# Optimization experiments

Measured on AMD Instinct MI355X. Metric: run time of the kernel, lower is better.

Reference implementation:

```python
import jax, jax.numpy as jnp
import numpy as np

N_NODES = 50000
N_EDGES = 800000
D_MODEL = 128
N_HEADS = 8
D_HEAD = D_MODEL // N_HEADS  # 16
BN_EPS = 1e-5


def _batch_norm(x, gamma, beta):
    # nn.BatchNorm1d in training mode: biased batch statistics over axis 0
    mean = jnp.mean(x, axis=0)
    var = jnp.mean((x - mean) ** 2, axis=0)
    return (x - mean) * jax.lax.rsqrt(var + BN_EPS) * gamma + beta


def setup_inputs() -> dict:
    key = jax.random.key(0)
    ks = jax.random.split(key, 20)
    s = 1.0 / np.sqrt(D_MODEL)
    inp = {
        "h": jax.random.normal(ks[0], (N_NODES, D_MODEL), jnp.float32),
        "p": jax.random.normal(ks[1], (N_NODES, 16), jnp.float32),
        "e": jax.random.normal(ks[2], (N_EDGES, D_MODEL), jnp.float32),
        # attention projections (use_bias=False)
        "Wq": jax.random.normal(ks[3], (D_MODEL, D_MODEL), jnp.float32) * s,
        "Wk": jax.random.normal(ks[4], (D_MODEL, D_MODEL), jnp.float32) * s,
        "We": jax.random.normal(ks[5], (D_MODEL, D_MODEL), jnp.float32) * s,
        "Wv": jax.random.normal(ks[6], (D_MODEL, D_MODEL), jnp.float32) * s,
        # output projection O_h (bias=True)
        "Wo": jax.random.normal(ks[7], (D_MODEL, D_MODEL), jnp.float32) * s,
        "bo": jnp.zeros((D_MODEL,), jnp.float32),
        # batch norms
        "bn1_g": jnp.ones((D_MODEL,), jnp.float32),
        "bn1_b": jnp.zeros((D_MODEL,), jnp.float32),
        "bn2_g": jnp.ones((D_MODEL,), jnp.float32),
        "bn2_b": jnp.zeros((D_MODEL,), jnp.float32),
        # FFN
        "W1": jax.random.normal(ks[8], (D_MODEL, 2 * D_MODEL), jnp.float32) * s,
        "b1": jnp.zeros((2 * D_MODEL,), jnp.float32),
        "W2": jax.random.normal(ks[9], (2 * D_MODEL, D_MODEL), jnp.float32) * (1.0 / np.sqrt(2 * D_MODEL)),
        "b2": jnp.zeros((D_MODEL,), jnp.float32),
        # edge list
        "src": jax.random.randint(ks[10], (N_EDGES,), 0, N_NODES, jnp.int32),
        "dst": jax.random.randint(ks[11], (N_EDGES,), 0, N_NODES, jnp.int32),
    }
    return inp


def reference(h, p, e, Wq, Wk, We, Wv, Wo, bo, bn1_g, bn1_b, bn2_g, bn2_b,
              W1, b1, W2, b2, src, dst):
    N = h.shape[0]
    # node/edge projections -> [N,H,D] / [E,H,D]
    Qh = (h @ Wq).reshape(N, N_HEADS, D_HEAD)
    Kh = (h @ Wk).reshape(N, N_HEADS, D_HEAD)
    Vh = (h @ Wv).reshape(N, N_HEADS, D_HEAD)
    Eh = (e @ We).reshape(-1, N_HEADS, D_HEAD)
    # per-edge score: (K[src] * Q[dst]) / sqrt(d) * E  -> [E,H,D]
    score = Kh[src] * Qh[dst] / np.sqrt(D_HEAD)
    score = score * Eh
    # clamped exp of per-head sum -> [E,H,1]
    s = jnp.exp(jnp.clip(jnp.sum(score, axis=-1, keepdims=True), -5.0, 5.0))
    # scatter-sum into destination nodes
    wV = jax.ops.segment_sum(Vh[src] * s, dst, num_segments=N)  # [N,H,D]
    z = jax.ops.segment_sum(s, dst, num_segments=N)             # [N,H,1]
    h_attn = (wV / (z + 1e-6)).reshape(N, D_MODEL)
    # output projection + residual + BN (dropout=0)
    h2 = h + (h_attn @ Wo + bo)
    h2 = _batch_norm(h2, bn1_g, bn1_b)
    # FFN + residual + BN
    ffn = jax.nn.relu(h2 @ W1 + b1) @ W2 + b2
    h3 = _batch_norm(h2 + ffn, bn2_g, bn2_b)
    return h3
```

## Files before the change

kernel.cpp:

```cpp
#include <hip/hip_runtime.h>

#define DM 128
#define NH 8
#define DH 16

typedef __bf16 bf8 __attribute__((ext_vector_type(8)));
typedef __bf16 bf4 __attribute__((ext_vector_type(4)));
typedef float  f4  __attribute__((ext_vector_type(4)));

__device__ __forceinline__ f4 mfma16(bf8 a, bf8 b, f4 c){
  return __builtin_amdgcn_mfma_f32_16x16x32_bf16(a, b, c, 0, 0, 0);
}

__device__ __forceinline__ bf8 bfragT(const __bf16* __restrict__ WT, int ldk, int lane){
  const __bf16* p = WT + (size_t)(lane & 15) * ldk + ((lane >> 4) << 3);
  return *(const bf8*)p;
}

__device__ __forceinline__ bf8 cvt8(const float* __restrict__ p){
  f4 u = *(const f4*)p;
  f4 v = *(const f4*)(p + 4);
  bf8 r;
  r[0]=(__bf16)u[0]; r[1]=(__bf16)u[1]; r[2]=(__bf16)u[2]; r[3]=(__bf16)u[3];
  r[4]=(__bf16)v[0]; r[5]=(__bf16)v[1]; r[6]=(__bf16)v[2]; r[7]=(__bf16)v[3];
  return r;
}

__global__ __launch_bounds__(256) void k_prep_hist(const float* __restrict__ Wq,
    const float* __restrict__ Wk, const float* __restrict__ Wv,
    const float* __restrict__ We, const float* __restrict__ Wo,
    const float* __restrict__ W1, const float* __restrict__ W2,
    __bf16* __restrict__ WqT, __bf16* __restrict__ WkT, __bf16* __restrict__ WvT,
    __bf16* __restrict__ WeT, __bf16* __restrict__ WoT,
    __bf16* __restrict__ W1T, __bf16* __restrict__ W2T,
    const int* __restrict__ dst, int* __restrict__ deg, int E)
{
  int b = blockIdx.x;
  if (b >= 576){
    int i = (b - 576) * 256 + threadIdx.x;
    if (i < E) atomicAdd(&deg[dst[i]], 1);
    return;
  }
  const float* W; __bf16* T; int K, M, idx;
  if (b < 320){
    int w = b >> 6;
    W = w==0?Wq: w==1?Wk: w==2?Wv: w==3?We: Wo;
    T = w==0?WqT: w==1?WkT: w==2?WvT: w==3?WeT: WoT;
    K = 128; M = 128; idx = (b & 63) * 256 + threadIdx.x;
  } else if (b < 448){
    W = W1; T = W1T; K = 128; M = 256; idx = (b - 320) * 256 + threadIdx.x;
  } else {
    W = W2; T = W2T; K = 256; M = 128; idx = (b - 448) * 256 + threadIdx.x;
  }
  int m = idx / K, k = idx - m * K;
  T[idx] = (__bf16)W[(size_t)k * M + m];
}

__global__ __launch_bounds__(256) void k_scanA(const int* __restrict__ deg,
    int* __restrict__ part, int N)
{
  __shared__ int ls[256];
  int b = blockIdx.x, t = threadIdx.x;
  int i = b * 256 + t;
  ls[t] = (i < N) ? deg[i] : 0;
  __syncthreads();
  for (int d = 128; d > 0; d >>= 1){
    if (t < d) ls[t] += ls[t + d];
    __syncthreads();
  }
  if (t == 0) part[b] = ls[0];
}

__global__ __launch_bounds__(256) void k_scanB(int* __restrict__ part, int nb)
{
  __shared__ int ls[256];
  int t = threadIdx.x;
  ls[t] = (t < nb) ? part[t] : 0;
  __syncthreads();
  for (int d = 1; d < 256; d <<= 1){
    int add = (t >= d) ? ls[t - d] : 0;
    __syncthreads();
    ls[t] += add;
    __syncthreads();
  }
  if (t < nb) part[t] = (t == 0) ? 0 : ls[t - 1];
}

__global__ __launch_bounds__(256) void k_scanC(const int* __restrict__ deg,
    const int* __restrict__ part, int* __restrict__ off, int* __restrict__ cursor, int N)
{
  __shared__ int ls[256];
  int b = blockIdx.x, t = threadIdx.x;
  int i = b * 256 + t;
  int v = (i < N) ? deg[i] : 0;
  ls[t] = v;
  __syncthreads();
  for (int d = 1; d < 256; d <<= 1){
    int add = (t >= d) ? ls[t - d] : 0;
    __syncthreads();
    ls[t] += add;
    __syncthreads();
  }
  if (i < N){
    int excl = ls[t] - v + part[b];
    off[i] = excl;
    cursor[i] = excl;
  }
}

__global__ __launch_bounds__(256) void k_qkv(const float* __restrict__ h,
    const __bf16* __restrict__ WqT, const __bf16* __restrict__ WkT, const __bf16* __restrict__ WvT,
    __bf16* __restrict__ Q, __bf16* __restrict__ K, __bf16* __restrict__ V, int N)
{
  int lane = threadIdx.x & 63;
  int r0 = (blockIdx.x * 4 + (threadIdx.x >> 6)) * 16;
  if (r0 + 16 > N) return;
  bf8 a[4];
  int arow = r0 + (lane & 15);
  int koff = (lane >> 4) << 3;
#pragma unroll
  for (int kt = 0; kt < 4; ++kt)
    a[kt] = cvt8(h + (size_t)arow * DM + kt * 32 + koff);

  const __bf16* Ws[3] = {WqT, WkT, WvT};
  __bf16* Os[3] = {Q, K, V};
  int crow = r0 + ((lane >> 4) << 2);
  int ccol = lane & 15;
#pragma unroll
  for (int o = 0; o < 3; ++o){
#pragma unroll
    for (int nt = 0; nt < 8; ++nt){
      f4 acc = {0.f, 0.f, 0.f, 0.f};
#pragma unroll
      for (int kt = 0; kt < 4; ++kt)
        acc = mfma16(a[kt], bfragT(Ws[o] + (size_t)(nt * 16) * DM + kt * 32, DM, lane), acc);
      __bf16* outp = Os[o] + (size_t)crow * DM + nt * 16 + ccol;
      outp[0] = (__bf16)acc[0]; outp[DM] = (__bf16)acc[1];
      outp[2 * DM] = (__bf16)acc[2]; outp[3 * DM] = (__bf16)acc[3];
    }
  }
}

__global__ __launch_bounds__(256) void k_edge(const float* __restrict__ e,
    const __bf16* __restrict__ WeT,
    const __bf16* __restrict__ Qb, const __bf16* __restrict__ Kb,
    const int* __restrict__ src, const int* __restrict__ dst,
    int* __restrict__ cursor, int* __restrict__ sSrc, float* __restrict__ sS,
    int E, int T, int NW)
{
  __shared__ __bf16 Eh[64][132];
  int tid = threadIdx.x, lane = tid & 63, wave = tid >> 6;
  int l16 = lane & 15;
  int koff = (lane >> 4) << 3;
  int half = lane >> 5, l32 = lane & 31, hh = l32 >> 2;
  int lrow = (lane >> 4) << 2;
  int wrow = wave * 16;
  int t = blockIdx.x * 4 + wave;
  if (t >= T) return;

  int ei = min(t * 16 + l16, E - 1);
  int sv = src[ei], dv = dst[ei];
  int slotv = 0;
  if ((lane < 16) && (t * 16 + l16 < E)){
    slotv = atomicAdd(&cursor[dv], 1);
    sSrc[slotv] = sv;
  }
  f4 eu[4], ew[4];
#pragma unroll
  for (int kt = 0; kt < 4; ++kt){
    const float* p = e + (size_t)ei * DM + kt * 32 + koff;
    eu[kt] = *(const f4*)p; ew[kt] = *(const f4*)(p + 4);
  }
  bf4 kr[8], qr[8];
#pragma unroll
  for (int i = 0; i < 8; ++i){
    int js = __shfl(sv, i * 2 + half, 64);
    int jd = __shfl(dv, i * 2 + half, 64);
    kr[i] = *(const bf4*)(Kb + (size_t)js * DM + l32 * 4);
    qr[i] = *(const bf4*)(Qb + (size_t)jd * DM + l32 * 4);
  }

  while (t < T){
    int tn = t + NW;
    bool hn = (tn < T);
    bf8 a[4];
#pragma unroll
    for (int kt = 0; kt < 4; ++kt){
      bf8 r;
      r[0]=(__bf16)eu[kt][0]; r[1]=(__bf16)eu[kt][1]; r[2]=(__bf16)eu[kt][2]; r[3]=(__bf16)eu[kt][3];
      r[4]=(__bf16)ew[kt][0]; r[5]=(__bf16)ew[kt][1]; r[6]=(__bf16)ew[kt][2]; r[7]=(__bf16)ew[kt][3];
      a[kt] = r;
    }
    int svn = 0, dvn = 0, slotn = 0;
    if (hn){
      int ein = min(tn * 16 + l16, E - 1);
      svn = src[ein]; dvn = dst[ein];
    }
#pragma unroll
    for (int nt = 0; nt < 8; ++nt){
      f4 acc = {0.f, 0.f, 0.f, 0.f};
#pragma unroll
      for (int kt = 0; kt < 4; ++kt)
        acc = mfma16(a[kt], bfragT(WeT + (size_t)(nt * 16) * DM + kt * 32, DM, lane), acc);
      int col = nt * 16 + l16;
#pragma unroll
      for (int r = 0; r < 4; ++r) Eh[wrow + lrow + r][col] = (__bf16)acc[r];
    }
    if (hn){
      int ern = min(tn * 16 + l16, E - 1);
#pragma unroll
      for (int kt = 0; kt < 4; ++kt){
        const float* p = e + (size_t)ern * DM + kt * 32 + koff;
        eu[kt] = *(const f4*)p; ew[kt] = *(const f4*)(p + 4);
      }
      if ((lane < 16) && (tn * 16 + l16 < E)){
        slotn = atomicAdd(&cursor[dvn], 1);
        sSrc[slotn] = svn;
      }
    }
    float ds[8];
#pragma unroll
    for (int q = 0; q < 8; ++q){
      bf4 evv = *(const bf4*)&Eh[wrow + q * 2 + half][l32 * 4];
      bf4 kv = kr[q], qv = qr[q];
      float d = (float)kv[0]*(float)qv[0]*(float)evv[0]
              + (float)kv[1]*(float)qv[1]*(float)evv[1]
              + (float)kv[2]*(float)qv[2]*(float)evv[2]
              + (float)kv[3]*(float)qv[3]*(float)evv[3];
      d += __shfl_xor(d, 1);
      d += __shfl_xor(d, 2);
      ds[q] = d;
    }
    if (hn){
#pragma unroll
      for (int i = 0; i < 8; ++i){
        int js = __shfl(svn, i * 2 + half, 64);
        int jd = __shfl(dvn, i * 2 + half, 64);
        kr[i] = *(const bf4*)(Kb + (size_t)js * DM + l32 * 4);
        qr[i] = *(const bf4*)(Qb + (size_t)jd * DM + l32 * 4);
      }
    }
    int jslot[8];
#pragma unroll
    for (int q = 0; q < 8; ++q) jslot[q] = __shfl(slotv, q * 2 + half, 64);
    if ((l32 & 3) == 0){
#pragma unroll
      for (int q = 0; q < 8; ++q){
        if ((t * 16 + q * 2 + half) < E){
          float dd = fminf(5.f, fmaxf(-5.f, ds[q] * 0.25f));
          sS[(size_t)jslot[q] * NH + hh] = __expf(dd);
        }
      }
    }
    sv = svn; dv = dvn; slotv = slotn;
    t = tn;
  }
}

__global__ __launch_bounds__(256) void k_gat_attnout(const int* __restrict__ off,
    const int* __restrict__ cend, const int* __restrict__ sSrc, const float* __restrict__ sS,
    const __bf16* __restrict__ Vb,
    const float* __restrict__ h, const __bf16* __restrict__ WoT, const float* __restrict__ bo,
    __bf16* __restrict__ h2, float* __restrict__ s1, float* __restrict__ s2, int N)
{
  __shared__ __bf16 hat[64][132];
  __shared__ float ls[256];
  int tid = threadIdx.x, lane = tid & 63, wave = tid >> 6;
  int half = lane >> 5, l32 = lane & 31, hh = l32 >> 2;
  int node0 = blockIdx.x * 64;
  ls[tid] = 0.f;

#pragma unroll 4
  for (int it = 0; it < 8; ++it){
    int local = wave * 16 + it * 2 + half;
    int node = node0 + local;
    int nodec = min(node, N - 1);
    int start = off[nodec], end = cend[nodec];
    float a0 = 0.f, a1 = 0.f, a2 = 0.f, a3 = 0.f, z = 0.f;
    for (int base = start; base < end; base += 8){
      int idx[8], sj[8]; float s[8];
#pragma unroll
      for (int q = 0; q < 8; ++q) idx[q] = min(base + q, end - 1);
#pragma unroll
      for (int q = 0; q < 8; ++q) sj[q] = sSrc[idx[q]];
#pragma unroll
      for (int q = 0; q < 8; ++q) s[q] = (base + q < end) ? sS[(size_t)idx[q] * NH + hh] : 0.f;
#pragma unroll
      for (int q = 0; q < 8; ++q){
        bf4 v = *(const bf4*)(Vb + (size_t)sj[q] * DM + l32 * 4);
        a0 += s[q] * (float)v[0]; a1 += s[q] * (float)v[1];
        a2 += s[q] * (float)v[2]; a3 += s[q] * (float)v[3];
        z += s[q];
      }
    }
    float invz = 1.f / (z + 1e-6f);
    bf4 o;
    o[0] = (__bf16)(a0 * invz); o[1] = (__bf16)(a1 * invz);
    o[2] = (__bf16)(a2 * invz); o[3] = (__bf16)(a3 * invz);
    *(bf4*)&hat[local][l32 * 4] = o;
  }
  __syncthreads();

  int r0 = node0 + wave * 16;
  bool active = (r0 + 16 <= N);
  int r0c = active ? r0 : 0;
  int kof = (lane >> 4) << 3;
  bf8 a[4];
#pragma unroll
  for (int kt = 0; kt < 4; ++kt)
    a[kt] = *(const bf8*)&hat[wave * 16 + (lane & 15)][kt * 32 + kof];
  int crow = r0c + ((lane >> 4) << 2);
  int ccol = lane & 15;
#pragma unroll
  for (int nt = 0; nt < 8; ++nt){
    f4 acc = {0.f, 0.f, 0.f, 0.f};
#pragma unroll
    for (int kt = 0; kt < 4; ++kt)
      acc = mfma16(a[kt], bfragT(WoT + (size_t)(nt * 16) * DM + kt * 32, DM, lane), acc);
    int col = nt * 16 + ccol;
    float bb = bo[col];
    if (active){
      float p1 = 0.f, p2 = 0.f;
#pragma unroll
      for (int r = 0; r < 4; ++r){
        size_t idx = (size_t)(crow + r) * DM + col;
        float v = h[idx] + acc[r] + bb;
        h2[idx] = (__bf16)v;
        p1 += v; p2 += v * v;
      }
      atomicAdd(&ls[col], p1);
      atomicAdd(&ls[128 + col], p2);
    }
  }
  __syncthreads();
  if (tid < 128){
    atomicAdd(&s1[tid], ls[tid]);
    atomicAdd(&s2[tid], ls[128 + tid]);
  }
}

__global__ __launch_bounds__(256) void k_ffn(const __bf16* __restrict__ h2,
    const float* __restrict__ s1a, const float* __restrict__ s2a,
    const float* __restrict__ g1, const float* __restrict__ be1,
    const __bf16* __restrict__ W1T, const float* __restrict__ b1,
    const __bf16* __restrict__ W2T, const float* __restrict__ b2,
    __bf16* __restrict__ y, float* __restrict__ s1, float* __restrict__ s2, int N)
{
  __shared__ __bf16 hid[4][16][264];
  __shared__ float ls[256];
  __shared__ float cls[128], clb[128];
  int tid = threadIdx.x;
  ls[tid] = 0.f;
  if (tid < 128){
    float mean = s1a[tid] / (float)N;
    float var  = s2a[tid] / (float)N - mean * mean;
    float rs   = rsqrtf(var + 1e-5f);
    float sc   = g1[tid] * rs;
    cls[tid] = sc;
    clb[tid] = be1[tid] - mean * sc;
  }
  __syncthreads();
  int lane = tid & 63, wave = tid >> 6;
  int r0 = (blockIdx.x * 4 + wave) * 16;
  bool active = (r0 + 16 <= N);
  int r0c = active ? r0 : 0;

  int arow = r0c + (lane & 15);
  int kof = (lane >> 4) << 3;
  bf8 a[4];
#pragma unroll
  for (int kt = 0; kt < 4; ++kt){
    int kb = kt * 32 + kof;
    bf8 hv = *(const bf8*)(h2 + (size_t)arow * DM + kb);
    bf8 r;
#pragma unroll
    for (int j = 0; j < 8; ++j)
      r[j] = (__bf16)((float)hv[j] * cls[kb + j] + clb[kb + j]);
    a[kt] = r;
  }
  int lr = (lane >> 4) << 2;
  int ccol = lane & 15;
#pragma unroll
  for (int nt = 0; nt < 16; ++nt){
    f4 acc = {0.f, 0.f, 0.f, 0.f};
#pragma unroll
    for (int kt = 0; kt < 4; ++kt)
      acc = mfma16(a[kt], bfragT(W1T + (size_t)(nt * 16) * DM + kt * 32, DM, lane), acc);
    int col = nt * 16 + ccol;
    float bb = b1[col];
#pragma unroll
    for (int r = 0; r < 4; ++r)
      hid[wave][lr + r][col] = (__bf16)fmaxf(acc[r] + bb, 0.f);
  }
  __syncthreads();
  f4 acc2[8];
#pragma unroll
  for (int nt = 0; nt < 8; ++nt){ acc2[nt][0]=0.f; acc2[nt][1]=0.f; acc2[nt][2]=0.f; acc2[nt][3]=0.f; }
#pragma unroll
  for (int kt = 0; kt < 8; ++kt){
    bf8 a2 = *(const bf8*)&hid[wave][lane & 15][kt * 32 + kof];
#pragma unroll
    for (int nt = 0; nt < 8; ++nt)
      acc2[nt] = mfma16(a2, bfragT(W2T + (size_t)(nt * 16) * 256 + kt * 32, 256, lane), acc2[nt]);
  }
  int crow = r0c + lr;
#pragma unroll
  for (int nt = 0; nt < 8; ++nt){
    int col = nt * 16 + ccol;
    float bb = b2[col], sc = cls[col], sb = clb[col];
    if (active){
      float p1 = 0.f, p2 = 0.f;
#pragma unroll
      for (int r = 0; r < 4; ++r){
        size_t idx = (size_t)(crow + r) * DM + col;
        float xres = (float)h2[idx] * sc + sb;
        float v = acc2[nt][r] + bb + xres;
        __bf16 vb = (__bf16)v;
        y[idx] = vb;
        float vr = (float)vb;
        p1 += vr; p2 += vr * vr;
      }
      atomicAdd(&ls[col], p1);
      atomicAdd(&ls[128 + col], p2);
    }
  }
  __syncthreads();
  if (tid < 128){
    atomicAdd(&s1[tid], ls[tid]);
    atomicAdd(&s2[tid], ls[128 + tid]);
  }
}

__global__ __launch_bounds__(256) void k_bnapply(const __bf16* __restrict__ y,
    float* __restrict__ out,
    const float* __restrict__ s1, const float* __restrict__ s2,
    const float* __restrict__ gam, const float* __restrict__ bet,
    int N, long long total4)
{
  __shared__ float cs[128], cb[128];
  int tid = threadIdx.x;
  if (tid < 128){
    float mean = s1[tid] / (float)N;
    float var  = s2[tid] / (float)N - mean * mean;
    float rs   = rsqrtf(var + 1e-5f);
    float sc   = gam[tid] * rs;
    cs[tid] = sc;
    cb[tid] = bet[tid] - mean * sc;
  }
  __syncthreads();
  long long i = (long long)blockIdx.x * blockDim.x + tid;
  if (i >= total4) return;
  bf4 v = *((const bf4*)y + i);
  int c = (int)((i * 4) & (DM - 1));
  f4 o;
  o[0] = (float)v[0] * cs[c]     + cb[c];
  o[1] = (float)v[1] * cs[c + 1] + cb[c + 1];
  o[2] = (float)v[2] * cs[c + 2] + cb[c + 2];
  o[3] = (float)v[3] * cs[c + 3] + cb[c + 3];
  *((f4*)out + i) = o;
}

extern "C" void kernel_launch(void* const* d_in, const int* in_sizes, int n_in,
                              void* d_out, int out_size, void* d_ws, size_t ws_size,
                              hipStream_t stream)
{
  const float* h    = (const float*)d_in[0];
  const float* e    = (const float*)d_in[2];
  const float* Wq   = (const float*)d_in[3];
  const float* Wk   = (const float*)d_in[4];
  const float* We   = (const float*)d_in[5];
  const float* Wv   = (const float*)d_in[6];
  const float* Wo   = (const float*)d_in[7];
  const float* bo   = (const float*)d_in[8];
  const float* bn1g = (const float*)d_in[9];
  const float* bn1b = (const float*)d_in[10];
  const float* bn2g = (const float*)d_in[11];
  const float* bn2b = (const float*)d_in[12];
  const float* W1   = (const float*)d_in[13];
  const float* b1   = (const float*)d_in[14];
  const float* W2   = (const float*)d_in[15];
  const float* b2   = (const float*)d_in[16];
  const int*   src  = (const int*)d_in[17];
  const int*   dst  = (const int*)d_in[18];

  int N = in_sizes[0] / DM;
  int E = in_sizes[2] / DM;
  float* out = (float*)d_out;

  char* ws = (char*)d_ws;
  size_t off_b = 0;
  auto alloc = [&](size_t bytes) -> char* {
    char* r = ws + off_b;
    off_b += (bytes + 255) & ~(size_t)255;
    return r;
  };
  __bf16* Qb    = (__bf16*)alloc((size_t)N * DM * 2);
  __bf16* Kb    = (__bf16*)alloc((size_t)N * DM * 2);
  __bf16* Vb    = (__bf16*)alloc((size_t)N * DM * 2);
  __bf16* h2    = (__bf16*)alloc((size_t)N * DM * 2);
  __bf16* y     = (__bf16*)alloc((size_t)N * DM * 2);
  int*   deg    = (int*)alloc((size_t)N * 4);
  int*   offs   = (int*)alloc((size_t)N * 4);
  int*   cursor = (int*)alloc((size_t)N * 4);
  int*   part   = (int*)alloc(256 * 4);
  int*   sSrc   = (int*)alloc((size_t)E * 4);
  float* sS     = (float*)alloc((size_t)E * NH * 4);
  float* stats = (float*)alloc(512 * 4);
  float* s1a = stats, *s2a = stats + 128, *s1b = stats + 256, *s2b = stats + 384;
  __bf16* WqT = (__bf16*)alloc(16384 * 2);
  __bf16* WkT = (__bf16*)alloc(16384 * 2);
  __bf16* WvT = (__bf16*)alloc(16384 * 2);
  __bf16* WeT = (__bf16*)alloc(16384 * 2);
  __bf16* WoT = (__bf16*)alloc(16384 * 2);
  __bf16* W1T = (__bf16*)alloc(32768 * 2);
  __bf16* W2T = (__bf16*)alloc(32768 * 2);

  hipMemsetAsync(deg, 0, (size_t)N * 4, stream);
  hipMemsetAsync(stats, 0, 512 * 4, stream);

  int histblocks = (E + 255) / 256;
  k_prep_hist<<<576 + histblocks, 256, 0, stream>>>(Wq, Wk, Wv, We, Wo, W1, W2,
      WqT, WkT, WvT, WeT, WoT, W1T, W2T, dst, deg, E);
  int scb = (N + 255) / 256;
  k_scanA<<<scb, 256, 0, stream>>>(deg, part, N);
  k_scanB<<<1, 256, 0, stream>>>(part, scb);
  k_scanC<<<scb, 256, 0, stream>>>(deg, part, offs, cursor, N);

  int rowblocks = (N / 16 + 3) / 4;
  k_qkv<<<rowblocks, 256, 0, stream>>>(h, WqT, WkT, WvT, Qb, Kb, Vb, N);
  int T = (E + 15) / 16;
  int eblocks = 2048;
  int NW = eblocks * 4;
  k_edge<<<eblocks, 256, 0, stream>>>(e, WeT, Qb, Kb, src, dst, cursor, sSrc, sS, E, T, NW);
  k_gat_attnout<<<(N + 63) / 64, 256, 0, stream>>>(offs, cursor, sSrc, sS, Vb,
      h, WoT, bo, h2, s1a, s2a, N);
  k_ffn<<<rowblocks, 256, 0, stream>>>(h2, s1a, s2a, bn1g, bn1b, W1T, b1, W2T, b2,
                                       y, s1b, s2b, N);
  long long total4 = (long long)N * DM / 4;
  k_bnapply<<<(int)((total4 + 255) / 256), 256, 0, stream>>>(y, out, s1b, s2b, bn2g, bn2b, N, total4);
}
```

Baseline: 446.9 us.

## Split fused attention gather and output projection into two kernels

The fused kernel that gathered weighted V rows per destination node and then ran the Wo MFMA projection is split in two. A gather kernel handles two nodes per wave with one node per half-wave across many more blocks, and writes h_attn as bf16 to global memory. A separate kernel reads it back for the projection and BN1 statistics. This is meant to expose more parallelism and latency hiding in the irregular gather, at the cost of an extra N×128 bf16 round trip through memory and one more launch.

```diff
diff --git a/kernel.cpp b/kernel.cpp
--- a/kernel.cpp
+++ b/kernel.cpp
@@ -257,58 +257,59 @@
   }
 }
 
-__global__ __launch_bounds__(256) void k_gat_attnout(const int* __restrict__ off,
+__global__ __launch_bounds__(256) void k_gather(const int* __restrict__ off,
     const int* __restrict__ cend, const int* __restrict__ sSrc, const float* __restrict__ sS,
-    const __bf16* __restrict__ Vb,
-    const float* __restrict__ h, const __bf16* __restrict__ WoT, const float* __restrict__ bo,
+    const __bf16* __restrict__ Vb, __bf16* __restrict__ hattn, int N)
+{
+  int lane = threadIdx.x & 63;
+  int half = lane >> 5, l32 = lane & 31;
+  int node = blockIdx.x * 8 + (threadIdx.x >> 6) * 2 + half;
+  if (node >= N) return;
+  int start = off[node], end = cend[node];
+  int hh = l32 >> 2;
+  float a0 = 0.f, a1 = 0.f, a2 = 0.f, a3 = 0.f, z = 0.f;
+  for (int base = start; base < end; base += 8){
+    int idx[8], sj[8]; float s[8];
+#pragma unroll
+    for (int q = 0; q < 8; ++q) idx[q] = min(base + q, end - 1);
+#pragma unroll
+    for (int q = 0; q < 8; ++q) sj[q] = sSrc[idx[q]];
+#pragma unroll
+    for (int q = 0; q < 8; ++q) s[q] = (base + q < end) ? sS[(size_t)idx[q] * NH + hh] : 0.f;
+#pragma unroll
+    for (int q = 0; q < 8; ++q){
+      bf4 v = *(const bf4*)(Vb + (size_t)sj[q] * DM + l32 * 4);
+      a0 += s[q] * (float)v[0]; a1 += s[q] * (float)v[1];
+      a2 += s[q] * (float)v[2]; a3 += s[q] * (float)v[3];
+      z += s[q];
+    }
+  }
+  float invz = 1.f / (z + 1e-6f);
+  bf4 o;
+  o[0] = (__bf16)(a0 * invz); o[1] = (__bf16)(a1 * invz);
+  o[2] = (__bf16)(a2 * invz); o[3] = (__bf16)(a3 * invz);
+  *(bf4*)(hattn + (size_t)node * DM + l32 * 4) = o;
+}
+
+__global__ __launch_bounds__(256) void k_attnout(const __bf16* __restrict__ hattn,
+    const float* __restrict__ h,
+    const __bf16* __restrict__ WoT, const float* __restrict__ bo,
     __bf16* __restrict__ h2, float* __restrict__ s1, float* __restrict__ s2, int N)
 {
-  __shared__ __bf16 hat[64][132];
   __shared__ float ls[256];
-  int tid = threadIdx.x, lane = tid & 63, wave = tid >> 6;
-  int half = lane >> 5, l32 = lane & 31, hh = l32 >> 2;
-  int node0 = blockIdx.x * 64;
+  int tid = threadIdx.x;
   ls[tid] = 0.f;
-
-#pragma unroll 4
-  for (int it = 0; it < 8; ++it){
-    int local = wave * 16 + it * 2 + half;
-    int node = node0 + local;
-    int nodec = min(node, N - 1);
-    int start = off[nodec], end = cend[nodec];
-    float a0 = 0.f, a1 = 0.f, a2 = 0.f, a3 = 0.f, z = 0.f;
-    for (int base = start; base < end; base += 8){
-      int idx[8], sj[8]; float s[8];
-#pragma unroll
-      for (int q = 0; q < 8; ++q) idx[q] = min(base + q, end - 1);
-#pragma unroll
-      for (int q = 0; q < 8; ++q) sj[q] = sSrc[idx[q]];
-#pragma unroll
-      for (int q = 0; q < 8; ++q) s[q] = (base + q < end) ? sS[(size_t)idx[q] * NH + hh] : 0.f;
-#pragma unroll
-      for (int q = 0; q < 8; ++q){
-        bf4 v = *(const bf4*)(Vb + (size_t)sj[q] * DM + l32 * 4);
-        a0 += s[q] * (float)v[0]; a1 += s[q] * (float)v[1];
-        a2 += s[q] * (float)v[2]; a3 += s[q] * (float)v[3];
-        z += s[q];
-      }
-    }
-    float invz = 1.f / (z + 1e-6f);
-    bf4 o;
-    o[0] = (__bf16)(a0 * invz); o[1] = (__bf16)(a1 * invz);
-    o[2] = (__bf16)(a2 * invz); o[3] = (__bf16)(a3 * invz);
-    *(bf4*)&hat[local][l32 * 4] = o;
-  }
-  __syncthreads();
-
-  int r0 = node0 + wave * 16;
+  __syncthreads();
+  int lane = tid & 63;
+  int r0 = (blockIdx.x * 4 + (tid >> 6)) * 16;
   bool active = (r0 + 16 <= N);
   int r0c = active ? r0 : 0;
+  int arow = r0c + (lane & 15);
   int kof = (lane >> 4) << 3;
   bf8 a[4];
 #pragma unroll
   for (int kt = 0; kt < 4; ++kt)
-    a[kt] = *(const bf8*)&hat[wave * 16 + (lane & 15)][kt * 32 + kof];
+    a[kt] = *(const bf8*)(hattn + (size_t)arow * DM + kt * 32 + kof);
   int crow = r0c + ((lane >> 4) << 2);
   int ccol = lane & 15;
 #pragma unroll
@@ -497,6 +498,7 @@
   __bf16* Qb    = (__bf16*)alloc((size_t)N * DM * 2);
   __bf16* Kb    = (__bf16*)alloc((size_t)N * DM * 2);
   __bf16* Vb    = (__bf16*)alloc((size_t)N * DM * 2);
+  __bf16* hattn = (__bf16*)alloc((size_t)N * DM * 2);
   __bf16* h2    = (__bf16*)alloc((size_t)N * DM * 2);
   __bf16* y     = (__bf16*)alloc((size_t)N * DM * 2);
   int*   deg    = (int*)alloc((size_t)N * 4);
@@ -532,8 +534,8 @@
   int eblocks = 2048;
   int NW = eblocks * 4;
   k_edge<<<eblocks, 256, 0, stream>>>(e, WeT, Qb, Kb, src, dst, cursor, sSrc, sS, E, T, NW);
-  k_gat_attnout<<<(N + 63) / 64, 256, 0, stream>>>(offs, cursor, sSrc, sS, Vb,
-      h, WoT, bo, h2, s1a, s2a, N);
+  k_gather<<<(N + 7) / 8, 256, 0, stream>>>(offs, cursor, sSrc, sS, Vb, hattn, N);
+  k_attnout<<<rowblocks, 256, 0, stream>>>(hattn, h, WoT, bo, h2, s1a, s2a, N);
   k_ffn<<<rowblocks, 256, 0, stream>>>(h2, s1a, s2a, bn1g, bn1b, W1T, b1, W2T, b2,
                                        y, s1b, s2b, N);
   long long total4 = (long long)N * DM / 4;
```

New measurement: 453.3 us. Within noise of the previous version (+1.4%).
